# Performance work log

Measured on AMD Instinct MI355X. Metric: run time of the kernel, lower is better.

## Reference

```python
import jax, jax.numpy as jnp
import numpy as np

VOCAB = 32000; D_MODEL = 768; N_LAYERS = 4
D_STATE = 16; D_CONV = 4; EXPAND = 2
D_INNER = EXPAND * D_MODEL                 # 1536
DT_RANK = (D_MODEL + 15) // 16             # 48
BATCH = 2; SEQ = 1024


def setup_inputs():
    key = jax.random.key(0)
    ks = jax.random.split(key, 10)
    def nrm(k, shape, scale=0.02):
        return (jax.random.normal(k, shape) * scale).astype(jnp.float32)
    inp = {}
    inp['tokens'] = jax.random.randint(ks[0], (BATCH, SEQ), 0, VOCAB)
    inp['embedding'] = nrm(ks[1], (VOCAB, D_MODEL))
    inp['head_bias'] = jnp.zeros((VOCAB,), jnp.float32)
    inp['ln_g'] = jnp.ones((N_LAYERS, D_MODEL), jnp.float32)
    inp['ln_b'] = jnp.zeros((N_LAYERS, D_MODEL), jnp.float32)
    inp['W_in'] = nrm(ks[2], (N_LAYERS, 2 * D_INNER, D_MODEL))
    inp['conv_w'] = nrm(ks[3], (N_LAYERS, D_INNER, 1, D_CONV), 0.1)
    inp['conv_b'] = jnp.zeros((N_LAYERS, D_INNER), jnp.float32)
    inp['W_xproj'] = nrm(ks[4], (N_LAYERS, DT_RANK + 2 * D_STATE, D_INNER))
    inp['W_dt'] = nrm(ks[5], (N_LAYERS, D_INNER, DT_RANK), 0.1)
    inp['b_dt'] = nrm(ks[6], (N_LAYERS, D_INNER), 0.5)
    # S4D-real init: A_n = n for n in 1..d_state
    inp['A_log'] = jnp.broadcast_to(jnp.log(jnp.arange(1, D_STATE + 1, dtype=jnp.float32)), (N_LAYERS, D_INNER, D_STATE)).copy()
    inp['D_ssm'] = jnp.ones((N_LAYERS, D_INNER), jnp.float32)
    inp['W_out'] = nrm(ks[7], (N_LAYERS, D_MODEL, D_INNER))
    inp['norm_g'] = jnp.ones((D_MODEL,), jnp.float32)
    inp['norm_b'] = jnp.zeros((D_MODEL,), jnp.float32)
    return inp


def _ln(x, g, b):
    m = jnp.mean(x, axis=-1, keepdims=True)
    v = jnp.var(x, axis=-1, keepdims=True)
    return (x - m) * jax.lax.rsqrt(v + 1e-5) * g + b


def _mamba(x, W_in, conv_w, conv_b, W_xproj, W_dt, b_dt, A_log, D_ssm, W_out):
    # x: (S, B, D_MODEL)
    xz = jnp.einsum('sbd,ed->sbe', x, W_in)           # (S, B, 2*D_INNER)
    xc, z = jnp.split(xz, 2, axis=-1)
    # depthwise causal conv along sequence
    xt = jnp.transpose(xc, (1, 2, 0))                  # (B, C, S)
    xt = jax.lax.conv_general_dilated(xt, conv_w, (1,), [(D_CONV - 1, 0)],
                                      dimension_numbers=('NCH', 'OIH', 'NCH'),
                                      feature_group_count=D_INNER)
    xt = xt + conv_b[None, :, None]
    xc = jax.nn.silu(jnp.transpose(xt, (2, 0, 1)))     # (S, B, C)
    xdb = jnp.einsum('sbc,ec->sbe', xc, W_xproj)       # (S, B, DT_RANK+2N)
    dt_r = xdb[..., :DT_RANK]
    Bm = xdb[..., DT_RANK:DT_RANK + D_STATE]
    Cm = xdb[..., DT_RANK + D_STATE:]
    dt = jax.nn.softplus(jnp.einsum('sbr,cr->sbc', dt_r, W_dt) + b_dt)
    A = -jnp.exp(A_log)                                # (C, N)

    def step(h, t):
        dt_t, B_t, C_t, x_t = t                        # (B,C),(B,N),(B,N),(B,C)
        dA = jnp.exp(dt_t[..., None] * A)              # (B, C, N)
        h = h * dA + (dt_t * x_t)[..., None] * B_t[:, None, :]
        y = jnp.einsum('bcn,bn->bc', h, C_t)
        return h, y

    h0 = jnp.zeros((x.shape[1], D_INNER, D_STATE), x.dtype)
    _, ys = jax.lax.scan(step, h0, (dt, Bm, Cm, xc))   # ys: (S, B, C)
    y = (ys + D_ssm * xc) * jax.nn.silu(z)
    return jnp.einsum('sbc,dc->sbd', y, W_out)


def reference(tokens, embedding, head_bias, ln_g, ln_b, W_in, conv_w, conv_b, W_xproj, W_dt, b_dt, A_log, D_ssm, W_out, norm_g, norm_b):
    x = embedding[tokens.T]                            # (S, B, D)
    for i in range(N_LAYERS):
        x = x + _mamba(_ln(x, ln_g[i], ln_b[i]), W_in[i], conv_w[i], conv_b[i],
                       W_xproj[i], W_dt[i], b_dt[i], A_log[i], D_ssm[i], W_out[i])
    x = _ln(x, norm_g, norm_b)
    logits = jnp.einsum('sbd,vd->sbv', x, embedding) + head_bias  # tied head
    return jnp.transpose(logits, (1, 0, 2))            # (B, S, VOCAB)
```

## Files before the change

kernel.cpp:

```cpp
#include <hip/hip_runtime.h>
#include <hip/hip_bf16.h>
#include <cstdint>
#include <cstddef>

#define SEQ_LEN 1024
#define NBATCH  2
#define MROWS   2048
#define DMODEL  768
#define DINNER  1536
#define DTRANK  48
#define DSTATE  16
#define NLAYERS 4
#define NVOCAB  32000
#define XPROJ_N 80
#define NCHUNK  16
#define CHUNK   64
#define GROUPS  (NBATCH * DINNER)
#define SCANW   (GROUPS * DSTATE)
#define XSPLIT  8

typedef __attribute__((ext_vector_type(4))) float f32x4;
typedef __attribute__((ext_vector_type(8))) short s16x8;
using bf16 = __hip_bfloat16;

__device__ __forceinline__ float b2f(bf16 v){ return __bfloat162float(v); }
__device__ __forceinline__ bf16  f2b(float v){ return __float2bfloat16(v); }
__device__ __forceinline__ short f2bs(float v){
  return (short)__builtin_bit_cast(unsigned short, __float2bfloat16(v));
}

__device__ __forceinline__ void glds16(const ushort* g, ushort* l) {
  __builtin_amdgcn_global_load_lds(
      (const __attribute__((address_space(1))) void*)g,
      (__attribute__((address_space(3))) void*)l,
      16, 0, 0);
}

#define CVT_E0 6144000
#define CVT_E1 (CVT_E0 + 2359296)
#define CVT_E2 (CVT_E1 + 1179648)
#define CVT_E3 (CVT_E2 + 122880)
#define CVT_E4 (CVT_E3 + 73728)
__global__ __launch_bounds__(256) void k_cvt5(
    const float* __restrict__ s0, const float* __restrict__ s1,
    const float* __restrict__ s2, const float* __restrict__ s3,
    const float* __restrict__ s4,
    ushort* __restrict__ d0, ushort* __restrict__ d1,
    ushort* __restrict__ d2, ushort* __restrict__ d3,
    ushort* __restrict__ d4)
{
  int i = blockIdx.x * 256 + threadIdx.x;
  const float* s; ushort* d; int base;
  if      (i < CVT_E0) { s = s0; d = d0; base = 0; }
  else if (i < CVT_E1) { s = s1; d = d1; base = CVT_E0; }
  else if (i < CVT_E2) { s = s2; d = d2; base = CVT_E1; }
  else if (i < CVT_E3) { s = s3; d = d3; base = CVT_E2; }
  else if (i < CVT_E4) { s = s4; d = d4; base = CVT_E3; }
  else return;
  int li = i - base;
  f32x4 v = *(const f32x4*)(s + (size_t)li * 4);
  ushort4 o;
  o.x = (ushort)f2bs(v[0]); o.y = (ushort)f2bs(v[1]);
  o.z = (ushort)f2bs(v[2]); o.w = (ushort)f2bs(v[3]);
  *(ushort4*)(d + (size_t)li * 4) = o;
}

__global__ __launch_bounds__(256) void k_xsum(const float* __restrict__ p,
    ushort* __restrict__ out, int n4) {
  int i = blockIdx.x * 256 + threadIdx.x;
  if (i >= n4) return;
  f32x4 s = {};
#pragma unroll
  for (int z = 0; z < XSPLIT; z++) {
    f32x4 v = *(const f32x4*)(p + (size_t)z * (MROWS * XPROJ_N) + (size_t)i * 4);
    s[0] += v[0]; s[1] += v[1]; s[2] += v[2]; s[3] += v[3];
  }
  ushort4 o;
  o.x = (ushort)f2bs(s[0]); o.y = (ushort)f2bs(s[1]);
  o.z = (ushort)f2bs(s[2]); o.w = (ushort)f2bs(s[3]);
  *(ushort4*)(out + (size_t)i * 4) = o;
}

__device__ __forceinline__ void ln_rows(const float v0[3], int t,
    const float* __restrict__ g, const float* __restrict__ b,
    bf16* __restrict__ outrow) {
  float s = 0.f, s2 = 0.f;
#pragma unroll
  for (int j = 0; j < 3; j++) { s += v0[j]; s2 += v0[j] * v0[j]; }
#pragma unroll
  for (int o = 32; o >= 1; o >>= 1) { s += __shfl_xor(s, o); s2 += __shfl_xor(s2, o); }
  __shared__ float red[8];
  int wave = t >> 6;
  if ((t & 63) == 0) { red[wave] = s; red[4 + wave] = s2; }
  __syncthreads();
  s  = red[0] + red[1] + red[2] + red[3];
  s2 = red[4] + red[5] + red[6] + red[7];
  float mean = s * (1.f / DMODEL);
  float var  = s2 * (1.f / DMODEL) - mean * mean;
  float rstd = rsqrtf(var + 1e-5f);
#pragma unroll
  for (int j = 0; j < 3; j++) {
    int d = t + j * 256;
    outrow[d] = f2b((v0[j] - mean) * rstd * g[d] + b[d]);
  }
}

__global__ __launch_bounds__(256) void k_ln(const float* __restrict__ x,
    bf16* __restrict__ out, const float* __restrict__ g, const float* __restrict__ b) {
  int m = blockIdx.x;
  const float* row = x + (size_t)m * DMODEL;
  int t = threadIdx.x;
  float v0[3];
#pragma unroll
  for (int j = 0; j < 3; j++) v0[j] = row[t + j * 256];
  ln_rows(v0, t, g, b, out + (size_t)m * DMODEL);
}

__global__ __launch_bounds__(256) void k_embed_ln(const int* __restrict__ tok,
    const float* __restrict__ emb, float* __restrict__ x,
    bf16* __restrict__ out, const float* __restrict__ g, const float* __restrict__ b) {
  int m = blockIdx.x;
  const float* row = emb + (size_t)tok[m] * DMODEL;
  int t = threadIdx.x;
  float v0[3];
#pragma unroll
  for (int j = 0; j < 3; j++) {
    v0[j] = row[t + j * 256];
    x[(size_t)m * DMODEL + t + j * 256] = v0[j];
  }
  ln_rows(v0, t, g, b, out + (size_t)m * DMODEL);
}

template<bool HAS_BIAS, int OMODE>
__global__ __launch_bounds__(512, 4) void k_gemm128(
    const ushort* __restrict__ A, int lda,
    const ushort* __restrict__ B, int ldb,
    void* __restrict__ C, int ldc,
    const float* __restrict__ bias,
    int M, int N, int K)
{
  __shared__ ushort As[2][128 * 32];
  __shared__ ushort Bs[2][128 * 32];
  const int t = threadIdx.x;
  const int lane = t & 63;
  const int wave = t >> 6;
  const int tile_m = blockIdx.x * 128;
  const int tile_n = blockIdx.y * 128;
  const int kper = K / gridDim.z;
  const int kb = blockIdx.z * kper;
  const int ke = kb + kper;
  const int wr = (wave >> 1) * 32;
  const int wc = (wave & 1) * 64;

  f32x4 acc[2][4] = {};

  const int sr = wave * 16 + (lane >> 2);
  const int sc = (lane & 3) * 8;
  const ushort* gA = A + (size_t)(tile_m + sr) * lda + sc + kb;
  const ushort* gB = B + (size_t)(tile_n + sr) * ldb + sc + kb;

  const int fr = lane & 15;
  const int kk = (lane >> 4) * 8;

  auto stage = [&](int bb) {
    glds16(gA, &As[bb][wave * 512]);
    glds16(gB, &Bs[bb][wave * 512]);
    gA += 32; gB += 32;
  };

  stage(0);
  int cur = 0;

  for (int k0 = kb; k0 < ke; k0 += 32) {
    if (k0 + 32 < ke) {
      stage(cur ^ 1);
      asm volatile("s_waitcnt vmcnt(2)" ::: "memory");
    } else {
      asm volatile("s_waitcnt vmcnt(0)" ::: "memory");
    }
    __builtin_amdgcn_s_barrier();

    s16x8 a[2], b[4];
#pragma unroll
    for (int m = 0; m < 2; m++)
      a[m] = *(const s16x8*)&As[cur][(wr + m * 16 + fr) * 32 + kk];
#pragma unroll
    for (int n = 0; n < 4; n++)
      b[n] = *(const s16x8*)&Bs[cur][(wc + n * 16 + fr) * 32 + kk];
#pragma unroll
    for (int m = 0; m < 2; m++)
#pragma unroll
      for (int n = 0; n < 4; n++)
        acc[m][n] = __builtin_amdgcn_mfma_f32_16x16x32_bf16(a[m], b[n], acc[m][n], 0, 0, 0);

    __builtin_amdgcn_s_barrier();
    cur ^= 1;
  }

  const int rq = (lane >> 4) * 4;
#pragma unroll
  for (int m = 0; m < 2; m++)
#pragma unroll
    for (int n = 0; n < 4; n++) {
      int colg = tile_n + wc + n * 16 + fr;
      float bv = HAS_BIAS ? bias[colg] : 0.f;
#pragma unroll
      for (int r = 0; r < 4; r++) {
        int rowg = tile_m + wr + m * 16 + rq + r;
        size_t idx = (size_t)rowg * ldc + colg;
        float v = acc[m][n][r] + bv;
        if constexpr (OMODE == 0) ((float*)C)[idx] = v;
        else if constexpr (OMODE == 1) atomicAdd((float*)C + idx, v);
        else ((bf16*)C)[idx] = f2b(v);
      }
    }
}

template<bool HAS_BIAS>
__global__ __launch_bounds__(512, 4) void k_gemmbig(
    const ushort* __restrict__ A, int lda,
    const ushort* __restrict__ B, int ldb,
    float* __restrict__ C, int ldc,
    const float* __restrict__ bias,
    int M, int N, int K)
{
  __shared__ ushort As[2][256 * 32];
  __shared__ ushort Bs[2][128 * 32];
  const int t = threadIdx.x;
  const int lane = t & 63;
  const int wave = t >> 6;
  const int tile_m = blockIdx.x * 256;
  const int tile_n = blockIdx.y * 128;
  const int wr = (wave >> 1) * 64;
  const int wc = (wave & 1) * 64;

  f32x4 acc[4][4] = {};

  const int sr = wave * 16 + (lane >> 2);
  const int sc = (lane & 3) * 8;
  const ushort* gA0 = A + (size_t)(tile_m + sr) * lda + sc;
  const ushort* gA1 = A + (size_t)(tile_m + 128 + sr) * lda + sc;
  const ushort* gB  = B + (size_t)(tile_n + sr) * ldb + sc;

  const int fr = lane & 15;
  const int kk = (lane >> 4) * 8;

  auto stage = [&](int bb) {
    glds16(gA0, &As[bb][wave * 512]);
    glds16(gA1, &As[bb][4096 + wave * 512]);
    glds16(gB,  &Bs[bb][wave * 512]);
    gA0 += 32; gA1 += 32; gB += 32;
  };

  stage(0);
  int cur = 0;

  for (int k0 = 0; k0 < K; k0 += 32) {
    if (k0 + 32 < K) {
      stage(cur ^ 1);
      asm volatile("s_waitcnt vmcnt(3)" ::: "memory");
    } else {
      asm volatile("s_waitcnt vmcnt(0)" ::: "memory");
    }
    __builtin_amdgcn_s_barrier();

    s16x8 a[4], b[4];
#pragma unroll
    for (int m = 0; m < 4; m++)
      a[m] = *(const s16x8*)&As[cur][(wr + m * 16 + fr) * 32 + kk];
#pragma unroll
    for (int n = 0; n < 4; n++)
      b[n] = *(const s16x8*)&Bs[cur][(wc + n * 16 + fr) * 32 + kk];
#pragma unroll
    for (int m = 0; m < 4; m++)
#pragma unroll
      for (int n = 0; n < 4; n++)
        acc[m][n] = __builtin_amdgcn_mfma_f32_16x16x32_bf16(a[m], b[n], acc[m][n], 0, 0, 0);

    __builtin_amdgcn_s_barrier();
    cur ^= 1;
  }

  const int rq = (lane >> 4) * 4;
#pragma unroll
  for (int m = 0; m < 4; m++)
#pragma unroll
    for (int n = 0; n < 4; n++) {
      int colg = tile_n + wc + n * 16 + fr;
      float bv = HAS_BIAS ? bias[colg] : 0.f;
#pragma unroll
      for (int r = 0; r < 4; r++) {
        int rowg = tile_m + wr + m * 16 + rq + r;
        C[(size_t)rowg * ldc + colg] = acc[m][n][r] + bv;
      }
    }
}

template<int MODE>
__global__ __launch_bounds__(256) void k_gemm(
    const ushort* __restrict__ A, int lda,
    const ushort* __restrict__ W, int ldw,
    void* __restrict__ Cout, int ldc,
    int M, int N, int K,
    const float* __restrict__ bias,
    const bf16* __restrict__ xcb,
    bf16* __restrict__ dtxp)
{
  __shared__ ushort As[64][40];
  __shared__ ushort Ws[64][40];
  const int tile_m = blockIdx.x * 64;
  const int tile_n = blockIdx.y * 64;
  const int t = threadIdx.x;
  const int lane = t & 63;
  const int wave = t >> 6;
  const int wr = (wave >> 1) * 32;
  const int wc = (wave & 1) * 32;
  f32x4 acc[2][2] = {};

  const int kper = ((K + gridDim.z - 1) / gridDim.z + 31) & ~31;
  const int kb = blockIdx.z * kper;
  int ke = kb + kper; if (ke > K) ke = K;

  const int srow = t >> 2;
  const int scol = (t & 3) * 8;

  for (int k0 = kb; k0 < ke; k0 += 32) {
    {
      int gm = tile_m + srow, gk = k0 + scol;
      s16x8 v = {};
      if (gm < M) {
        if (gk + 8 <= K) v = *(const s16x8*)(A + (size_t)gm * lda + gk);
        else {
#pragma unroll
          for (int j = 0; j < 8; j++) if (gk + j < K) v[j] = (short)A[(size_t)gm * lda + gk + j];
        }
      }
      *(s16x8*)&As[srow][scol] = v;
    }
    {
      int gn = tile_n + srow, gk = k0 + scol;
      s16x8 v = {};
      if (gn < N) {
        if (gk + 8 <= K) v = *(const s16x8*)(W + (size_t)gn * ldw + gk);
        else {
#pragma unroll
          for (int j = 0; j < 8; j++) if (gk + j < K) v[j] = (short)W[(size_t)gn * ldw + gk + j];
        }
      }
      *(s16x8*)&Ws[srow][scol] = v;
    }
    __syncthreads();
    const int kk = (lane >> 4) * 8;
    const int fr = lane & 15;
    s16x8 a0 = *(const s16x8*)&As[wr + fr][kk];
    s16x8 a1 = *(const s16x8*)&As[wr + 16 + fr][kk];
    s16x8 b0 = *(const s16x8*)&Ws[wc + fr][kk];
    s16x8 b1 = *(const s16x8*)&Ws[wc + 16 + fr][kk];
    acc[0][0] = __builtin_amdgcn_mfma_f32_16x16x32_bf16(a0, b0, acc[0][0], 0, 0, 0);
    acc[0][1] = __builtin_amdgcn_mfma_f32_16x16x32_bf16(a0, b1, acc[0][1], 0, 0, 0);
    acc[1][0] = __builtin_amdgcn_mfma_f32_16x16x32_bf16(a1, b0, acc[1][0], 0, 0, 0);
    acc[1][1] = __builtin_amdgcn_mfma_f32_16x16x32_bf16(a1, b1, acc[1][1], 0, 0, 0);
    __syncthreads();
  }

  const int fr = lane & 15;
  const int rq = (lane >> 4) * 4;
#pragma unroll
  for (int i = 0; i < 2; i++)
#pragma unroll
    for (int j = 0; j < 2; j++) {
      int colg = tile_n + wc + j * 16 + fr;
#pragma unroll
      for (int r = 0; r < 4; r++) {
        int rowg = tile_m + wr + i * 16 + rq + r;
        if (rowg < M && colg < N) {
          float v = acc[i][j][r];
          size_t idx = (size_t)rowg * ldc + colg;
          if constexpr (MODE == 0) {
            ((bf16*)Cout)[idx] = f2b(v);
          } else if constexpr (MODE == 2) {
            v += bias[colg];
            float sp = (v > 20.f) ? v : log1pf(__expf(v));
            ((float*)Cout)[idx] = sp;
            dtxp[idx] = f2b(sp * b2f(xcb[idx]));
          } else {
            ((float*)Cout)[(size_t)blockIdx.z * (MROWS * XPROJ_N) + idx] = v;
          }
        }
      }
    }
}

__global__ __launch_bounds__(256) void k_conv(const bf16* __restrict__ xz,
    const float* __restrict__ w, const float* __restrict__ cb,
    bf16* __restrict__ xcb) {
  int id = blockIdx.x * 256 + threadIdx.x;
  int m = id / DINNER, c = id - m * DINNER;
  int s = m & (SEQ_LEN - 1);
  float acc = cb[c];
#pragma unroll
  for (int k = 0; k < 4; k++) {
    int sp = s - 3 + k;
    if (sp >= 0) acc += w[c * 4 + k] * b2f(xz[(size_t)(m - 3 + k) * (2 * DINNER) + c]);
  }
  float sil = acc / (1.f + __expf(-acc));
  xcb[id] = f2b(sil);
}

__global__ __launch_bounds__(256) void k_scan(const float* __restrict__ dt,
    const bf16* __restrict__ dtx, const bf16* __restrict__ xdb,
    const float* __restrict__ A_log, bf16* __restrict__ y) {
  int cb = blockIdx.x;
  int c = cb % DINNER, b = cb / DINNER;
  int t = threadIdx.x;
  int n = t & 15, j = t >> 4;
  float Acn = -__expf(A_log[c * DSTATE + n]);
  int mbase = b * SEQ_LEN + j * CHUNK;

  float h = 0.f, ap = 1.f;
#pragma unroll 4
  for (int s = 0; s < CHUNK; s++) {
    int m = mbase + s;
    float dtv = dt[(size_t)m * DINNER + c];
    float dxv = b2f(dtx[(size_t)m * DINNER + c]);
    float Bv  = b2f(xdb[(size_t)m * XPROJ_N + DTRANK + n]);
    float dA  = __expf(dtv * Acn);
    h = h * dA + dxv * Bv;
    ap *= dA;
  }

  __shared__ float Ap[NCHUNK][DSTATE + 1];
  __shared__ float He[NCHUNK][DSTATE + 1];
  __shared__ float Hin[NCHUNK][DSTATE + 1];
  Ap[j][n] = ap; He[j][n] = h;
  __syncthreads();
  if (t < DSTATE) {
    float hh = 0.f;
#pragma unroll
    for (int jj = 0; jj < NCHUNK; jj++) {
      Hin[jj][t] = hh;
      hh = Ap[jj][t] * hh + He[jj][t];
    }
  }
  __syncthreads();

  h = Hin[j][n];
#pragma unroll 2
  for (int s = 0; s < CHUNK; s++) {
    int m = mbase + s;
    float dtv = dt[(size_t)m * DINNER + c];
    float dxv = b2f(dtx[(size_t)m * DINNER + c]);
    float Bv  = b2f(xdb[(size_t)m * XPROJ_N + DTRANK + n]);
    float Cv  = b2f(xdb[(size_t)m * XPROJ_N + DTRANK + DSTATE + n]);
    float dA  = __expf(dtv * Acn);
    h = h * dA + dxv * Bv;
    float p = h * Cv;
    p += __shfl_xor(p, 8);
    p += __shfl_xor(p, 4);
    p += __shfl_xor(p, 2);
    p += __shfl_xor(p, 1);
    if (n == 0) y[(size_t)m * DINNER + c] = f2b(p);
  }
}

__global__ __launch_bounds__(256) void k_ycomb(const bf16* __restrict__ y,
    const bf16* __restrict__ xcb, const bf16* __restrict__ xz,
    const float* __restrict__ D_ssm, bf16* __restrict__ ybf) {
  int id = blockIdx.x * 256 + threadIdx.x;
  int m = id / DINNER, c = id - m * DINNER;
  float z = b2f(xz[(size_t)m * (2 * DINNER) + DINNER + c]);
  float sil = z / (1.f + __expf(-z));
  float v = (b2f(y[id]) + D_ssm[c] * b2f(xcb[id])) * sil;
  ybf[id] = f2b(v);
}

extern "C" void kernel_launch(void* const* d_in, const int* in_sizes, int n_in,
                              void* d_out, int out_size, void* d_ws, size_t ws_size,
                              hipStream_t stream) {
  const int*   tokens    = (const int*)  d_in[0];
  const float* embedding = (const float*)d_in[1];
  const float* head_bias = (const float*)d_in[2];
  const float* ln_g      = (const float*)d_in[3];
  const float* ln_b      = (const float*)d_in[4];
  const float* W_in      = (const float*)d_in[5];
  const float* conv_w    = (const float*)d_in[6];
  const float* conv_b    = (const float*)d_in[7];
  const float* W_xproj   = (const float*)d_in[8];
  const float* W_dt      = (const float*)d_in[9];
  const float* b_dt      = (const float*)d_in[10];
  const float* A_log     = (const float*)d_in[11];
  const float* D_ssm     = (const float*)d_in[12];
  const float* W_out     = (const float*)d_in[13];
  const float* norm_g    = (const float*)d_in[14];
  const float* norm_b    = (const float*)d_in[15];
  float* out = (float*)d_out;

  char* ws = (char*)d_ws;
  size_t off = 0;
  auto alloc = [&](size_t bytes) -> char* {
    char* p = ws + off;
    off = (off + bytes + 255) & ~(size_t)255;
    return p;
  };
  float*  x     = (float*) alloc((size_t)MROWS * DMODEL * 4);
  bf16*   xln   = (bf16*)  alloc((size_t)MROWS * DMODEL * 2);
  bf16*   xz    = (bf16*)  alloc((size_t)MROWS * 2 * DINNER * 2);
  bf16*   xcb   = (bf16*)  alloc((size_t)MROWS * DINNER * 2);
  bf16*   xdb   = (bf16*)  alloc((size_t)MROWS * XPROJ_N * 2);
  float*  xdbp  = (float*) alloc((size_t)XSPLIT * MROWS * XPROJ_N * 4);
  float*  dtf   = (float*) alloc((size_t)MROWS * DINNER * 4);
  bf16*   dtx   = (bf16*)  alloc((size_t)MROWS * DINNER * 2);
  bf16*   yraw  = (bf16*)  alloc((size_t)MROWS * DINNER * 2);
  bf16*   ybf   = (bf16*)  alloc((size_t)MROWS * DINNER * 2);
  ushort* ebf   = (ushort*)alloc((size_t)NVOCAB * DMODEL * 2);
  ushort* winb  = (ushort*)alloc((size_t)NLAYERS * 2 * DINNER * DMODEL * 2);
  ushort* wxpb  = (ushort*)alloc((size_t)NLAYERS * XPROJ_N * DINNER * 2);
  ushort* wdtb  = (ushort*)alloc((size_t)NLAYERS * DINNER * DTRANK * 2);
  ushort* woutb = (ushort*)alloc((size_t)NLAYERS * DMODEL * DINNER * 2);
  (void)ws_size; (void)in_sizes; (void)n_in; (void)out_size;

  k_cvt5<<<(CVT_E4 + 255) / 256, 256, 0, stream>>>(
      embedding, W_in, W_out, W_xproj, W_dt,
      ebf, winb, woutb, wxpb, wdtb);

  k_embed_ln<<<MROWS, 256, 0, stream>>>(tokens, embedding, x, xln, ln_g, ln_b);

  const int XDBN4 = MROWS * XPROJ_N / 4;

  for (int L = 0; L < NLAYERS; L++) {
    if (L > 0)
      k_ln<<<MROWS, 256, 0, stream>>>(x, xln, ln_g + L * DMODEL, ln_b + L * DMODEL);

    k_gemm128<false, 2><<<dim3(MROWS / 128, (2 * DINNER) / 128), 512, 0, stream>>>(
        (const ushort*)xln, DMODEL,
        winb + (size_t)L * 2 * DINNER * DMODEL, DMODEL,
        (void*)xz, 2 * DINNER, nullptr, MROWS, 2 * DINNER, DMODEL);

    k_conv<<<MROWS * DINNER / 256, 256, 0, stream>>>(
        xz, conv_w + (size_t)L * DINNER * 4, conv_b + (size_t)L * DINNER, xcb);

    k_gemm<3><<<dim3(MROWS / 64, 2, XSPLIT), 256, 0, stream>>>(
        (const ushort*)xcb, DINNER,
        wxpb + (size_t)L * XPROJ_N * DINNER, DINNER,
        (void*)xdbp, XPROJ_N, MROWS, XPROJ_N, DINNER,
        nullptr, nullptr, nullptr);
    k_xsum<<<(XDBN4 + 255) / 256, 256, 0, stream>>>(xdbp, (ushort*)xdb, XDBN4);

    k_gemm<2><<<dim3(MROWS / 64, DINNER / 64), 256, 0, stream>>>(
        (const ushort*)xdb, XPROJ_N,
        wdtb + (size_t)L * DINNER * DTRANK, DTRANK,
        (void*)dtf, DINNER, MROWS, DINNER, DTRANK,
        b_dt + (size_t)L * DINNER, xcb, dtx);

    k_scan<<<GROUPS, 256, 0, stream>>>(
        dtf, dtx, xdb, A_log + (size_t)L * DINNER * DSTATE, yraw);

    k_ycomb<<<MROWS * DINNER / 256, 256, 0, stream>>>(
        yraw, xcb, xz, D_ssm + (size_t)L * DINNER, ybf);

    k_gemm128<false, 1><<<dim3(MROWS / 128, DMODEL / 128, 4), 512, 0, stream>>>(
        (const ushort*)ybf, DINNER,
        woutb + (size_t)L * DMODEL * DINNER, DINNER,
        (void*)x, DMODEL, nullptr, MROWS, DMODEL, DINNER);
  }

  k_ln<<<MROWS, 256, 0, stream>>>(x, xln, norm_g, norm_b);

  k_gemmbig<true><<<dim3(MROWS / 256, NVOCAB / 128), 512, 0, stream>>>(
      (const ushort*)xln, DMODEL,
      ebf, DMODEL,
      out, NVOCAB, head_bias, MROWS, NVOCAB, DMODEL);
}
```

Before: 1.093 ms.

## Split chunked scan into three kernels and swizzle head GEMM tile order

The chunked selective scan, previously one block per (batch, channel) with an in-block shared-memory carry pass, is split into three kernels. The first computes per-chunk decay products and end states, the second propagates carries across chunks, and the third recomputes the scan with the carried-in state. Thread mapping changes so consecutive threads span different channels within a chunk, which aims for coalesced loads of dt and dtx instead of strided per-channel access. Separately, the big vocab-head GEMM remaps block IDs so the eight blocks scheduled together cover all M tiles of one N column, improving L2 reuse of the embedding tile. The cost is extra launches and global-memory traffic for the intermediate state arrays, and the swizzle hardcodes eight M tiles.

New measurement: 967.1 us. 1.13x faster.

```diff
diff --git a/kernel.cpp b/kernel.cpp
--- a/kernel.cpp
+++ b/kernel.cpp
@@ -229,8 +229,13 @@
   const int t = threadIdx.x;
   const int lane = t & 63;
   const int wave = t >> 6;
-  const int tile_m = blockIdx.x * 256;
-  const int tile_n = blockIdx.y * 128;
+
+  const int orig = blockIdx.y * gridDim.x + blockIdx.x;
+  const int q = (gridDim.x * gridDim.y) >> 3;
+  const int tid = (orig & 7) * q + (orig >> 3);
+  const int tile_m = (tid & 7) * 256;
+  const int tile_n = (tid >> 3) * 128;
+
   const int wr = (wave >> 1) * 64;
   const int wc = (wave & 1) * 64;
 
@@ -407,17 +412,20 @@
   xcb[id] = f2b(sil);
 }
 
-__global__ __launch_bounds__(256) void k_scan(const float* __restrict__ dt,
+__global__ __launch_bounds__(256) void k_scan1(const float* __restrict__ dt,
     const bf16* __restrict__ dtx, const bf16* __restrict__ xdb,
-    const float* __restrict__ A_log, bf16* __restrict__ y) {
-  int cb = blockIdx.x;
-  int c = cb % DINNER, b = cb / DINNER;
-  int t = threadIdx.x;
-  int n = t & 15, j = t >> 4;
+    const float* __restrict__ A_log, float* __restrict__ aprod,
+    float* __restrict__ hend) {
+  int gid = blockIdx.x * 256 + threadIdx.x;
+  int n  = gid & 15;
+  int t2 = gid >> 4;
+  int j  = t2 / GROUPS;
+  int cb = t2 - j * GROUPS;
+  int c  = cb % DINNER;
+  int b  = cb / DINNER;
   float Acn = -__expf(A_log[c * DSTATE + n]);
+  float h = 0.f, ap = 1.f;
   int mbase = b * SEQ_LEN + j * CHUNK;
-
-  float h = 0.f, ap = 1.f;
 #pragma unroll 4
   for (int s = 0; s < CHUNK; s++) {
     int m = mbase + s;
@@ -428,23 +436,35 @@
     h = h * dA + dxv * Bv;
     ap *= dA;
   }
-
-  __shared__ float Ap[NCHUNK][DSTATE + 1];
-  __shared__ float He[NCHUNK][DSTATE + 1];
-  __shared__ float Hin[NCHUNK][DSTATE + 1];
-  Ap[j][n] = ap; He[j][n] = h;
-  __syncthreads();
-  if (t < DSTATE) {
-    float hh = 0.f;
-#pragma unroll
-    for (int jj = 0; jj < NCHUNK; jj++) {
-      Hin[jj][t] = hh;
-      hh = Ap[jj][t] * hh + He[jj][t];
-    }
-  }
-  __syncthreads();
-
-  h = Hin[j][n];
+  aprod[gid] = ap;
+  hend[gid]  = h;
+}
+
+__global__ __launch_bounds__(256) void k_scan2(const float* __restrict__ aprod,
+    const float* __restrict__ hend, float* __restrict__ hin) {
+  int idx = blockIdx.x * 256 + threadIdx.x;
+  float h = 0.f;
+#pragma unroll
+  for (int j = 0; j < NCHUNK; j++) {
+    hin[(size_t)j * SCANW + idx] = h;
+    h = aprod[(size_t)j * SCANW + idx] * h + hend[(size_t)j * SCANW + idx];
+  }
+}
+
+__global__ __launch_bounds__(256) void k_scan3(const float* __restrict__ dt,
+    const bf16* __restrict__ dtx, const bf16* __restrict__ xdb,
+    const float* __restrict__ A_log, const float* __restrict__ hin,
+    bf16* __restrict__ y) {
+  int gid = blockIdx.x * 256 + threadIdx.x;
+  int n  = gid & 15;
+  int t2 = gid >> 4;
+  int j  = t2 / GROUPS;
+  int cb = t2 - j * GROUPS;
+  int c  = cb % DINNER;
+  int b  = cb / DINNER;
+  float Acn = -__expf(A_log[c * DSTATE + n]);
+  float h = hin[gid];
+  int mbase = b * SEQ_LEN + j * CHUNK;
 #pragma unroll 2
   for (int s = 0; s < CHUNK; s++) {
     int m = mbase + s;
@@ -512,6 +532,9 @@
   bf16*   dtx   = (bf16*)  alloc((size_t)MROWS * DINNER * 2);
   bf16*   yraw  = (bf16*)  alloc((size_t)MROWS * DINNER * 2);
   bf16*   ybf   = (bf16*)  alloc((size_t)MROWS * DINNER * 2);
+  float*  aprod = (float*) alloc((size_t)SCANW * NCHUNK * 4);
+  float*  hend  = (float*) alloc((size_t)SCANW * NCHUNK * 4);
+  float*  hin   = (float*) alloc((size_t)SCANW * NCHUNK * 4);
   ushort* ebf   = (ushort*)alloc((size_t)NVOCAB * DMODEL * 2);
   ushort* winb  = (ushort*)alloc((size_t)NLAYERS * 2 * DINNER * DMODEL * 2);
   ushort* wxpb  = (ushort*)alloc((size_t)NLAYERS * XPROJ_N * DINNER * 2);
@@ -552,8 +575,10 @@
         (void*)dtf, DINNER, MROWS, DINNER, DTRANK,
         b_dt + (size_t)L * DINNER, xcb, dtx);
 
-    k_scan<<<GROUPS, 256, 0, stream>>>(
-        dtf, dtx, xdb, A_log + (size_t)L * DINNER * DSTATE, yraw);
+    const float* Al = A_log + (size_t)L * DINNER * DSTATE;
+    k_scan1<<<SCANW * NCHUNK / 256, 256, 0, stream>>>(dtf, dtx, xdb, Al, aprod, hend);
+    k_scan2<<<SCANW / 256, 256, 0, stream>>>(aprod, hend, hin);
+    k_scan3<<<SCANW * NCHUNK / 256, 256, 0, stream>>>(dtf, dtx, xdb, Al, hin, yraw);
 
     k_ycomb<<<MROWS * DINNER / 256, 256, 0, stream>>>(
         yraw, xcb, xz, D_ssm + (size_t)L * DINNER, ybf);
```
